# Optimization experiments

Hardware: AMD Instinct MI355X
Metric: run time of the kernel (lower is better)

## Reference

```python
import jax, jax.numpy as jnp
import numpy as np

K = 6  # hardcoded top-k in the original forward


def setup_inputs() -> dict:
    key = jax.random.key(0)
    k1, k2, k3, k4, k5 = jax.random.split(key, 5)
    N, M, C = 512, 2048, 256
    return {
        "micro": jax.random.normal(k1, (N, C), jnp.float32),
        "label": jax.random.uniform(k2, (N,), jnp.float32),
        "micro_all": jax.random.normal(k3, (M, C), jnp.float32),
        "label_all": jax.random.uniform(k4, (M,), jnp.float32),
        # fc = nn.Linear(channels, 1, bias=False) -> weight vector [C]
        "fc_w": jax.random.normal(k5, (C,), jnp.float32) * 0.05,
    }


def reference(micro, label, micro_all, label_all, fc_w):
    N, C = micro.shape
    M = micro_all.shape[0]
    # Pairwise squared differences: dis[n, m, c] = (micro_all[m,c] - micro[n,c])^2
    dis = (micro_all[None, :, :] - micro[:, None, :]) ** 2  # [N, M, C]
    # Linear(C,1,bias=False) along channel dim, minus per-pair channel mean
    anti = jnp.einsum('nmc,c->nm', dis, fc_w) - dis.mean(axis=2)  # [N, M]
    anti = jax.nn.softmax(anti, axis=1)
    # top-k mask (argsort-based selection of k largest == lax.top_k)
    _, idx = jax.lax.top_k(anti, K)  # [N, K]
    mask = jnp.zeros((N, M), anti.dtype).at[jnp.arange(N)[:, None], idx].set(1.0)
    cut = anti * mask
    cut = cut / jnp.sum(cut, axis=1, keepdims=True)  # renormalize kNN weights
    micro_tmp = micro + cut @ micro_all  # [N, C]
    # composition loss
    dis_label = jnp.abs(label_all[None, :] - label[:, None])  # [N, M]
    co_loss = jnp.asarray(1e-4, cut.dtype) + jnp.sum(dis_label * cut) / N
    return micro_tmp, co_loss
```

## Files before the change

### kernel.cpp

```cpp
#include <hip/hip_runtime.h>
#include <hip/hip_bf16.h>
#include <math.h>

#define N_Q   512
#define M_ALL 2048
#define CHN   256
#define TOPK  6
#define INV_C (1.0f / 256.0f)

#define WS_LOSS  64
#define WS_LOGIT 4096

typedef __bf16 bf16x8 __attribute__((ext_vector_type(8)));
typedef float  f32x4  __attribute__((ext_vector_type(4)));

static __device__ __forceinline__ unsigned short bfbits(float x) {
    __bf16 h = (__bf16)x;
    unsigned short u;
    __builtin_memcpy(&u, &h, 2);
    return u;
}

#define BM 64
#define BN 32
#define LDK 264

__global__ __launch_bounds__(256) void gcn_gemm(
    const float* __restrict__ micro_all,
    const float* __restrict__ micro,
    const float* __restrict__ fc_w,
    float* __restrict__ logits)
{
    __shared__ unsigned short sA[BM][LDK];
    __shared__ unsigned short sB[BN][LDK];
    __shared__ float s_bias[BM];

    const int t    = threadIdx.x;
    const int w    = t >> 6;
    const int l15  = t & 15;
    const int quad = (t >> 4) & 3;
    const int m0   = blockIdx.x * BM;
    const int n0   = blockIdx.y * BN;

    const int rg = t >> 4;
    const int c0 = (t & 15) * 4;

    float4 wv[4];
    #pragma unroll
    for (int cc = 0; cc < 4; ++cc) {
        float4 x = *(const float4*)(fc_w + c0 + cc * 64);
        x.x -= INV_C; x.y -= INV_C; x.z -= INV_C; x.w -= INV_C;
        wv[cc] = x;
    }

    #pragma unroll
    for (int i = 0; i < 4; ++i) {
        const int r = i * 16 + rg;
        const float* rp = micro_all + (size_t)(m0 + r) * CHN;
        float p = 0.0f;
        #pragma unroll
        for (int cc = 0; cc < 4; ++cc) {
            const float4 v = *(const float4*)(rp + c0 + cc * 64);
            const float sx = v.x * wv[cc].x;
            const float sy = v.y * wv[cc].y;
            const float sz = v.z * wv[cc].z;
            const float sw = v.w * wv[cc].w;
            ushort4 pk;
            pk.x = bfbits(sx); pk.y = bfbits(sy); pk.z = bfbits(sz); pk.w = bfbits(sw);
            *(ushort4*)&sA[r][c0 + cc * 64] = pk;
            p += v.x * sx + v.y * sy + v.z * sz + v.w * sw;
        }
        #pragma unroll
        for (int mask = 8; mask >= 1; mask >>= 1)
            p += __shfl_xor(p, mask, 64);
        if ((t & 15) == 0) s_bias[r] = p;
    }

    #pragma unroll
    for (int i = 0; i < 2; ++i) {
        const int r = i * 16 + rg;
        const float* rp = micro + (size_t)(n0 + r) * CHN;
        #pragma unroll
        for (int cc = 0; cc < 4; ++cc) {
            const float4 v = *(const float4*)(rp + c0 + cc * 64);
            ushort4 pk;
            pk.x = bfbits(v.x); pk.y = bfbits(v.y); pk.z = bfbits(v.z); pk.w = bfbits(v.w);
            *(ushort4*)&sB[r][c0 + cc * 64] = pk;
        }
    }
    __syncthreads();

    const int nt    = w & 1;
    const int mtp   = w >> 1;
    const int rowB  = nt * 16 + l15;
    const int rowA0 = mtp * 32 + l15;
    const int rowA1 = mtp * 32 + 16 + l15;

    f32x4 acc0 = {0.f, 0.f, 0.f, 0.f};
    f32x4 acc1 = {0.f, 0.f, 0.f, 0.f};
    #pragma unroll
    for (int ks = 0; ks < 8; ++ks) {
        const int k0 = ks * 32 + quad * 8;
        const bf16x8 a  = *(const bf16x8*)&sB[rowB][k0];
        const bf16x8 b0 = *(const bf16x8*)&sA[rowA0][k0];
        const bf16x8 b1 = *(const bf16x8*)&sA[rowA1][k0];
        acc0 = __builtin_amdgcn_mfma_f32_16x16x32_bf16(a, b0, acc0, 0, 0, 0);
        acc1 = __builtin_amdgcn_mfma_f32_16x16x32_bf16(a, b1, acc1, 0, 0, 0);
    }

    const float bias0 = s_bias[mtp * 32 + l15];
    const float bias1 = s_bias[mtp * 32 + 16 + l15];
    #pragma unroll
    for (int reg = 0; reg < 4; ++reg) {
        const int n = n0 + nt * 16 + quad * 4 + reg;
        logits[(size_t)n * M_ALL + m0 + mtp * 32 + l15]      = bias0 - 2.f * acc0[reg];
        logits[(size_t)n * M_ALL + m0 + mtp * 32 + 16 + l15] = bias1 - 2.f * acc1[reg];
    }
}

#define BLOCK 256
#define WAVES (BLOCK / 64)
#define MPT   (M_ALL / BLOCK)
#define WTOP  8
#define NCAND (WAVES * WTOP)
#define NREF  10

static __device__ __forceinline__ unsigned key_of(float f, int m) {
    unsigned u = __float_as_uint(f);
    u = (u & 0x80000000u) ? ~u : (u | 0x80000000u);
    return (u & 0xFFFFF800u) | (unsigned)m;
}

__global__ __launch_bounds__(BLOCK) void gcn_topk(
    const float* __restrict__ logits,
    const float* __restrict__ micro,
    const float* __restrict__ label,
    const float* __restrict__ micro_all,
    const float* __restrict__ label_all,
    const float* __restrict__ fc_w,
    float* __restrict__ out,
    float* __restrict__ loss_arr)
{
    __shared__ unsigned s_keys[NCAND];
    __shared__ unsigned s_top[NREF];
    __shared__ float    s_ex[NREF];

    const int n    = blockIdx.x;
    const int t    = threadIdx.x;
    const int wave = t >> 6;
    const int lane = t & 63;

    const float4 b4 = *(const float4*)(micro + (size_t)n * CHN + lane * 4);
    float4 w4 = *(const float4*)(fc_w + lane * 4);
    w4.x -= INV_C; w4.y -= INV_C; w4.z -= INV_C; w4.w -= INV_C;

    unsigned k8[MPT];
    #pragma unroll
    for (int j = 0; j < MPT; ++j) {
        const int m = t + j * BLOCK;
        k8[j] = key_of(logits[(size_t)n * M_ALL + m], m);
    }

    #pragma unroll
    for (int k = 0; k < WTOP; ++k) {
        unsigned best = k8[0];
        #pragma unroll
        for (int j = 1; j < MPT; ++j) best = (k8[j] > best) ? k8[j] : best;
        #pragma unroll
        for (int mask = 32; mask > 0; mask >>= 1) {
            const unsigned ov = __shfl_xor(best, mask, 64);
            best = (ov > best) ? ov : best;
        }
        if (lane == 0) s_keys[wave * WTOP + k] = best;
        #pragma unroll
        for (int j = 0; j < MPT; ++j)
            k8[j] = (k8[j] == best) ? 0u : k8[j];
    }
    __syncthreads();

    {
        unsigned v = s_keys[lane & 31];
        #pragma unroll
        for (int k = 2; k <= 32; k <<= 1) {
            #pragma unroll
            for (int j = k >> 1; j >= 1; j >>= 1) {
                const unsigned pv = __shfl_xor(v, j, 64);
                const unsigned mx = (v > pv) ? v : pv;
                const unsigned mn = (v > pv) ? pv : v;
                const bool up    = ((lane & k) == 0);
                const bool lower = ((lane & j) == 0);
                v = (up == lower) ? mx : mn;
            }
        }
        if (wave == 0 && lane < NREF) s_top[lane] = v;
    }
    __syncthreads();

    for (int c = wave; c < NREF; c += WAVES) {
        const int m = (int)(s_top[c] & 0x7FFu);
        const float4 a = *(const float4*)(micro_all + (size_t)m * CHN + lane * 4);
        const float dx = a.x - b4.x;
        const float dy = a.y - b4.y;
        const float dz = a.z - b4.z;
        const float dw = a.w - b4.w;
        float acc = dx * dx * w4.x + dy * dy * w4.y + dz * dz * w4.z + dw * dw * w4.w;
        #pragma unroll
        for (int mask = 32; mask >= 1; mask >>= 1)
            acc += __shfl_xor(acc, mask, 64);
        if (lane == 0) s_ex[c] = acc;
    }
    __syncthreads();

    float top_val[TOPK];
    int   top_idx[TOPK];
    unsigned rtk = 0u;
    #pragma unroll
    for (int k = 0; k < TOPK; ++k) {
        float best = -INFINITY;
        int   bi   = 0;
        #pragma unroll
        for (int c = 0; c < NREF; ++c) {
            const bool avail = ((rtk >> c) & 1u) == 0u;
            const float cv = s_ex[c];
            if (avail && cv > best) { best = cv; bi = c; }
        }
        top_val[k] = best;
        top_idx[k] = (int)(s_top[bi] & 0x7FFu);
        rtk |= 1u << bi;
    }

    const float mx = top_val[0];
    float e[TOPK];
    float esum = 0.0f;
    #pragma unroll
    for (int k = 0; k < TOPK; ++k) { e[k] = __expf(top_val[k] - mx); esum += e[k]; }
    const float inv = 1.0f / esum;

    float outv = micro[(size_t)n * CHN + t];
    #pragma unroll
    for (int k = 0; k < TOPK; ++k)
        outv += (e[k] * inv) * micro_all[(size_t)top_idx[k] * CHN + t];
    out[n * CHN + t] = outv;

    if (t == 0) {
        const float lab = label[n];
        float l = 0.0f;
        #pragma unroll
        for (int k = 0; k < TOPK; ++k)
            l += (e[k] * inv) * fabsf(label_all[top_idx[k]] - lab);
        loss_arr[n] = l;
    }
}

__global__ __launch_bounds__(256) void gcn_finalize(
    const float* __restrict__ loss_arr,
    float* __restrict__ out)
{
    __shared__ float red[4];
    const int t = threadIdx.x;
    float v = loss_arr[t] + loss_arr[t + 256];
    #pragma unroll
    for (int mask = 32; mask >= 1; mask >>= 1)
        v += __shfl_xor(v, mask, 64);
    if ((t & 63) == 0) red[t >> 6] = v;
    __syncthreads();
    if (t == 0)
        out[N_Q * CHN] = 1e-4f + (red[0] + red[1] + red[2] + red[3]) / (float)N_Q;
}

extern "C" void kernel_launch(void* const* d_in, const int* in_sizes, int n_in,
                              void* d_out, int out_size, void* d_ws, size_t ws_size,
                              hipStream_t stream) {
    const float* micro     = (const float*)d_in[0];
    const float* label     = (const float*)d_in[1];
    const float* micro_all = (const float*)d_in[2];
    const float* label_all = (const float*)d_in[3];
    const float* fc_w      = (const float*)d_in[4];
    float* out    = (float*)d_out;
    float* ws     = (float*)d_ws;
    float* loss   = ws + WS_LOSS;
    float* logits = ws + WS_LOGIT;

    gcn_gemm<<<dim3(M_ALL / BM, N_Q / BN), 256, 0, stream>>>(
        micro_all, micro, fc_w, logits);
    gcn_topk<<<N_Q, BLOCK, 0, stream>>>(logits, micro, label, micro_all,
                                        label_all, fc_w, out, loss);
    gcn_finalize<<<1, 256, 0, stream>>>(loss, out);
}
```

Measured before the change: 78.36 us.

## Emit sort keys from GEMM, widen top-k blocks, fold loss reduction into atomics

The GEMM epilogue now writes packed sortable keys directly, so the top-k kernel no longer converts logits. The top-k kernel moves to 512-thread blocks with 4 candidates per thread, and a 64-wide bitonic sort runs in one wave. The separate finalize kernel is removed: the GEMM initialises the loss scalar and each row atomically adds its contribution, saving one launch. The trade-off is that floating-point atomics make the summation order nondeterministic, and the 512-thread blocks leave half the threads idle in the output phase.

```diff
diff --git a/kernel.cpp b/kernel.cpp
--- a/kernel.cpp
+++ b/kernel.cpp
@@ -8,8 +8,7 @@
 #define TOPK  6
 #define INV_C (1.0f / 256.0f)
 
-#define WS_LOSS  64
-#define WS_LOGIT 4096
+#define WS_KEYS 4096
 
 typedef __bf16 bf16x8 __attribute__((ext_vector_type(8)));
 typedef float  f32x4  __attribute__((ext_vector_type(4)));
@@ -21,6 +20,12 @@
     return u;
 }
 
+static __device__ __forceinline__ unsigned key_of(float f, int m) {
+    unsigned u = __float_as_uint(f);
+    u = (u & 0x80000000u) ? ~u : (u | 0x80000000u);
+    return (u & 0xFFFFF800u) | (unsigned)m;
+}
+
 #define BM 64
 #define BN 32
 #define LDK 264
@@ -29,7 +34,8 @@
     const float* __restrict__ micro_all,
     const float* __restrict__ micro,
     const float* __restrict__ fc_w,
-    float* __restrict__ logits)
+    unsigned* __restrict__ keys,
+    float* __restrict__ out)
 {
     __shared__ unsigned short sA[BM][LDK];
     __shared__ unsigned short sB[BN][LDK];
@@ -41,6 +47,9 @@
     const int quad = (t >> 4) & 3;
     const int m0   = blockIdx.x * BM;
     const int n0   = blockIdx.y * BN;
+
+    if (blockIdx.x == 0 && blockIdx.y == 0 && t == 0)
+        out[N_Q * CHN] = 1e-4f;
 
     const int rg = t >> 4;
     const int c0 = (t & 15) * 4;
@@ -110,38 +119,32 @@
 
     const float bias0 = s_bias[mtp * 32 + l15];
     const float bias1 = s_bias[mtp * 32 + 16 + l15];
+    const int   mA = m0 + mtp * 32 + l15;
+    const int   mB = mA + 16;
     #pragma unroll
     for (int reg = 0; reg < 4; ++reg) {
         const int n = n0 + nt * 16 + quad * 4 + reg;
-        logits[(size_t)n * M_ALL + m0 + mtp * 32 + l15]      = bias0 - 2.f * acc0[reg];
-        logits[(size_t)n * M_ALL + m0 + mtp * 32 + 16 + l15] = bias1 - 2.f * acc1[reg];
-    }
-}
-
-#define BLOCK 256
-#define WAVES (BLOCK / 64)
-#define MPT   (M_ALL / BLOCK)
-#define WTOP  8
-#define NCAND (WAVES * WTOP)
-#define NREF  10
-
-static __device__ __forceinline__ unsigned key_of(float f, int m) {
-    unsigned u = __float_as_uint(f);
-    u = (u & 0x80000000u) ? ~u : (u | 0x80000000u);
-    return (u & 0xFFFFF800u) | (unsigned)m;
-}
-
-__global__ __launch_bounds__(BLOCK) void gcn_topk(
-    const float* __restrict__ logits,
+        keys[(size_t)n * M_ALL + mA] = key_of(bias0 - 2.f * acc0[reg], mA);
+        keys[(size_t)n * M_ALL + mB] = key_of(bias1 - 2.f * acc1[reg], mB);
+    }
+}
+
+#define TBLOCK 512
+#define TWAVES (TBLOCK / 64)
+#define TMPT   (M_ALL / TBLOCK)
+#define TNCAND (TWAVES * 8)
+#define NREF   10
+
+__global__ __launch_bounds__(TBLOCK) void gcn_topk(
+    const unsigned* __restrict__ keys,
     const float* __restrict__ micro,
     const float* __restrict__ label,
     const float* __restrict__ micro_all,
     const float* __restrict__ label_all,
     const float* __restrict__ fc_w,
-    float* __restrict__ out,
-    float* __restrict__ loss_arr)
+    float* __restrict__ out)
 {
-    __shared__ unsigned s_keys[NCAND];
+    __shared__ unsigned s_keys[TNCAND];
     __shared__ unsigned s_top[NREF];
     __shared__ float    s_ex[NREF];
 
@@ -154,34 +157,32 @@
     float4 w4 = *(const float4*)(fc_w + lane * 4);
     w4.x -= INV_C; w4.y -= INV_C; w4.z -= INV_C; w4.w -= INV_C;
 
-    unsigned k8[MPT];
-    #pragma unroll
-    for (int j = 0; j < MPT; ++j) {
-        const int m = t + j * BLOCK;
-        k8[j] = key_of(logits[(size_t)n * M_ALL + m], m);
-    }
-
-    #pragma unroll
-    for (int k = 0; k < WTOP; ++k) {
-        unsigned best = k8[0];
-        #pragma unroll
-        for (int j = 1; j < MPT; ++j) best = (k8[j] > best) ? k8[j] : best;
+    unsigned k4[TMPT];
+    #pragma unroll
+    for (int j = 0; j < TMPT; ++j)
+        k4[j] = keys[(size_t)n * M_ALL + t + j * TBLOCK];
+
+    #pragma unroll
+    for (int k = 0; k < 8; ++k) {
+        unsigned best = k4[0];
+        #pragma unroll
+        for (int j = 1; j < TMPT; ++j) best = (k4[j] > best) ? k4[j] : best;
         #pragma unroll
         for (int mask = 32; mask > 0; mask >>= 1) {
             const unsigned ov = __shfl_xor(best, mask, 64);
             best = (ov > best) ? ov : best;
         }
-        if (lane == 0) s_keys[wave * WTOP + k] = best;
-        #pragma unroll
-        for (int j = 0; j < MPT; ++j)
-            k8[j] = (k8[j] == best) ? 0u : k8[j];
-    }
-    __syncthreads();
-
-    {
-        unsigned v = s_keys[lane & 31];
-        #pragma unroll
-        for (int k = 2; k <= 32; k <<= 1) {
+        if (lane == 0) s_keys[wave * 8 + k] = best;
+        #pragma unroll
+        for (int j = 0; j < TMPT; ++j)
+            k4[j] = (k4[j] == best) ? 0u : k4[j];
+    }
+    __syncthreads();
+
+    if (wave == 0) {
+        unsigned v = s_keys[lane];
+        #pragma unroll
+        for (int k = 2; k <= 64; k <<= 1) {
             #pragma unroll
             for (int j = k >> 1; j >= 1; j >>= 1) {
                 const unsigned pv = __shfl_xor(v, j, 64);
@@ -192,11 +193,11 @@
                 v = (up == lower) ? mx : mn;
             }
         }
-        if (wave == 0 && lane < NREF) s_top[lane] = v;
-    }
-    __syncthreads();
-
-    for (int c = wave; c < NREF; c += WAVES) {
+        if (lane < NREF) s_top[lane] = v;
+    }
+    __syncthreads();
+
+    for (int c = wave; c < NREF; c += TWAVES) {
         const int m = (int)(s_top[c] & 0x7FFu);
         const float4 a = *(const float4*)(micro_all + (size_t)m * CHN + lane * 4);
         const float dx = a.x - b4.x;
@@ -236,11 +237,13 @@
     for (int k = 0; k < TOPK; ++k) { e[k] = __expf(top_val[k] - mx); esum += e[k]; }
     const float inv = 1.0f / esum;
 
-    float outv = micro[(size_t)n * CHN + t];
-    #pragma unroll
-    for (int k = 0; k < TOPK; ++k)
-        outv += (e[k] * inv) * micro_all[(size_t)top_idx[k] * CHN + t];
-    out[n * CHN + t] = outv;
+    if (t < CHN) {
+        float outv = micro[(size_t)n * CHN + t];
+        #pragma unroll
+        for (int k = 0; k < TOPK; ++k)
+            outv += (e[k] * inv) * micro_all[(size_t)top_idx[k] * CHN + t];
+        out[n * CHN + t] = outv;
+    }
 
     if (t == 0) {
         const float lab = label[n];
@@ -248,24 +251,8 @@
         #pragma unroll
         for (int k = 0; k < TOPK; ++k)
             l += (e[k] * inv) * fabsf(label_all[top_idx[k]] - lab);
-        loss_arr[n] = l;
-    }
-}
-
-__global__ __launch_bounds__(256) void gcn_finalize(
-    const float* __restrict__ loss_arr,
-    float* __restrict__ out)
-{
-    __shared__ float red[4];
-    const int t = threadIdx.x;
-    float v = loss_arr[t] + loss_arr[t + 256];
-    #pragma unroll
-    for (int mask = 32; mask >= 1; mask >>= 1)
-        v += __shfl_xor(v, mask, 64);
-    if ((t & 63) == 0) red[t >> 6] = v;
-    __syncthreads();
-    if (t == 0)
-        out[N_Q * CHN] = 1e-4f + (red[0] + red[1] + red[2] + red[3]) / (float)N_Q;
+        atomicAdd(out + N_Q * CHN, l * (1.0f / (float)N_Q));
+    }
 }
 
 extern "C" void kernel_launch(void* const* d_in, const int* in_sizes, int n_in,
@@ -276,14 +263,11 @@
     const float* micro_all = (const float*)d_in[2];
     const float* label_all = (const float*)d_in[3];
     const float* fc_w      = (const float*)d_in[4];
-    float* out    = (float*)d_out;
-    float* ws     = (float*)d_ws;
-    float* loss   = ws + WS_LOSS;
-    float* logits = ws + WS_LOGIT;
+    float*    out  = (float*)d_out;
+    unsigned* keys = (unsigned*)((float*)d_ws + WS_KEYS);
 
     gcn_gemm<<<dim3(M_ALL / BM, N_Q / BN), 256, 0, stream>>>(
-        micro_all, micro, fc_w, logits);
-    gcn_topk<<<N_Q, BLOCK, 0, stream>>>(logits, micro, label, micro_all,
-                                        label_all, fc_w, out, loss);
-    gcn_finalize<<<1, 256, 0, stream>>>(loss, out);
-}
+        micro_all, micro, fc_w, keys, out);
+    gcn_topk<<<N_Q, TBLOCK, 0, stream>>>(keys, micro, label, micro_all,
+                                         label_all, fc_w, out);
+}
```

After: 82.40 us. +5.2%, slower.
